# Kernel tuning notes

Hardware: AMD Instinct MI355X
Metric: run time of the kernel (lower is better)

## Reference

```python
import jax, jax.numpy as jnp
import numpy as np

N_NODES = 50000
N_EDGES = 800000
D_IN = 128
D_HID = 128
D_OUT = 128
EPS = 0.1  # GINConv eps


def setup_inputs() -> dict:
    key = jax.random.key(0)
    k = jax.random.split(key, 8)
    scale = 1.0 / np.sqrt(D_IN)
    return {
        "x": jax.random.normal(k[0], (N_NODES, D_IN), dtype=jnp.float32),
        "edge_index": jax.random.randint(k[1], (2, N_EDGES), 0, N_NODES, dtype=jnp.int64),
        "edge_weight": jax.random.uniform(k[2], (N_EDGES,), dtype=jnp.float32),
        "W1a": jax.random.normal(k[3], (D_IN, D_HID), dtype=jnp.float32) * scale,
        "W1b": jax.random.normal(k[4], (D_HID, D_HID), dtype=jnpp.float32) if False else jax.random.normal(k[4], (D_HID, D_HID), dtype=jnp.float32) * scale,
        "W2a": jax.random.normal(k[5], (D_HID, D_HID), dtype=jnp.float32) * scale,
        "W2b": jax.random.normal(k[6], (D_HID, D_OUT), dtype=jnp.float32) * scale,
    }


def _gin_conv(h, src, dst, ew, Wa, Wb, n_nodes):
    # edge-weighted neighbor sum: aggr[i] = sum_{(j->i)} w_ji * h[j]
    msg = ew[:, None] * h[src]                       # [E, d]
    aggr = jax.ops.segment_sum(msg, dst, num_segments=n_nodes)  # [N, d]
    z = (1.0 + EPS) * h + aggr                       # GIN update
    # 2-layer bias-free MLP: lin -> relu -> lin
    return jnp.maximum(z @ Wa, 0.0) @ Wb


def reference(x, edge_index, edge_weight, W1a, W1b, W2a, W2b):
    src, dst = edge_index[0], edge_index[1]
    n = x.shape[0]
    h = _gin_conv(x, src, dst, edge_weight, W1a, W1b, n)
    h = jnp.maximum(h, 0.0)  # relu between convs; dropout is identity in eval
    h = _gin_conv(h, src, dst, edge_weight, W2a, W2b, n)
    return h
```

## Files before the change

kernel.cpp:

```cpp
#include <hip/hip_runtime.h>
#include <hip/hip_fp16.h>

#define D 128
#define N_NODES 50000
#define EPSP1 1.1f

#define NPB 256
#define NBUCK 196
#define CAP 5120
#define P1E 2048
#define TS 136

typedef __attribute__((ext_vector_type(8))) short short8;
typedef __attribute__((ext_vector_type(4))) float f32x4;

__device__ __forceinline__ unsigned short f2bf(float f) {
    unsigned u = __float_as_uint(f);
    u += 0x7FFF + ((u >> 16) & 1);
    return (unsigned short)(u >> 16);
}
__device__ __forceinline__ float bf2f(unsigned short h) {
    return __uint_as_float(((unsigned)h) << 16);
}

__global__ __launch_bounds__(256) void pass1_bucket(
    const int* __restrict__ src, const int* __restrict__ dst,
    const float* __restrict__ ew, int* __restrict__ gcnt,
    uint2* __restrict__ gstage, int ne)
{
    __shared__ int bcnt[NBUCK];
    __shared__ int goff[NBUCK];
    int tid = threadIdx.x;
    int bid = blockIdx.x;
    if (tid < NBUCK) bcnt[tid] = 0;
    __syncthreads();
    int e0 = bid * P1E;
    int   rank[8];
    int   buck[8];
    uint2 pay[8];
#pragma unroll
    for (int j = 0; j < 8; ++j) {
        int e = e0 + j * 256 + tid;
        buck[j] = -1;
        if (e < ne) {
            int d_ = dst[e];
            int b  = d_ >> 8;
            int dl = d_ & 255;
            pay[j].x = (unsigned)(src[e] & 0xFFFF) | ((unsigned)dl << 16);
            pay[j].y = (unsigned)__half_as_ushort(__float2half_rn(ew[e]));
            rank[j]  = atomicAdd(&bcnt[b], 1);
            buck[j]  = b;
        }
    }
    __syncthreads();
    if (tid < NBUCK && bcnt[tid] > 0)
        goff[tid] = atomicAdd(&gcnt[tid], bcnt[tid]);
    __syncthreads();
#pragma unroll
    for (int j = 0; j < 8; ++j) {
        if (buck[j] >= 0) {
            int pos = goff[buck[j]] + rank[j];
            if (pos < CAP)
                gstage[(size_t)buck[j] * CAP + pos] = pay[j];
        }
    }
}

__global__ __launch_bounds__(512) void fused_mid(
    const uint2* __restrict__ gstage, const int* __restrict__ gcnt,
    unsigned* __restrict__ epay, int* __restrict__ off,
    const float* __restrict__ x, unsigned short* __restrict__ hb, int n4,
    const float* __restrict__ W1a, const float* __restrict__ W1b,
    const float* __restrict__ W2a, const float* __restrict__ W2b,
    unsigned short* __restrict__ wp)
{
    __shared__ int hist[NPB];
    __shared__ int scn[NPB];
    __shared__ int loc[NPB];
    __shared__ int wtot[8];
    __shared__ int base_s;
    __shared__ unsigned csr[CAP];

    int bid = blockIdx.x;
    int t = threadIdx.x;

    if (bid < NBUCK) {
        int b = bid;
        int cnt = min(gcnt[b], CAP);

        if (t < NPB) hist[t] = 0;
        __syncthreads();

        uint2 ent[CAP / 512];
#pragma unroll
        for (int it = 0; it < CAP / 512; ++it) {
            int i = it * 512 + t;
            if (i < cnt) {
                ent[it] = gstage[(size_t)b * CAP + i];
                atomicAdd(&hist[(ent[it].x >> 16) & 255], 1);
            }
        }
        __syncthreads();

        int w = t >> 6, l = t & 63;
        if (w < 4) {
            int v = hist[w * 64 + l];
#pragma unroll
            for (int dd = 1; dd < 64; dd <<= 1) {
                int u = __shfl_up(v, dd, 64);
                if (l >= dd) v += u;
            }
            scn[w * 64 + l] = v;
            if (l == 63) wtot[w] = v;
        } else if (w == 4) {
            int v = 0;
            for (int i = l; i < NBUCK; i += 64)
                if (i < b) v += min(gcnt[i], CAP);
#pragma unroll
            for (int dd = 32; dd > 0; dd >>= 1) v += __shfl_down(v, dd, 64);
            if (l == 0) base_s = v;
        }
        __syncthreads();

        if (t < NPB) {
            int pre = 0;
#pragma unroll
            for (int j = 0; j < 3; ++j) if (j < w) pre += wtot[j];
            int incl = scn[t] + pre;
            int excl = incl - hist[t];
            int node = (b << 8) + t;
            if (node <= N_NODES) off[node] = base_s + excl;
            loc[t] = excl;
        }
        __syncthreads();

#pragma unroll
        for (int it = 0; it < CAP / 512; ++it) {
            int i = it * 512 + t;
            if (i < cnt) {
                int dl = (ent[it].x >> 16) & 255;
                int p = atomicAdd(&loc[dl], 1);
                csr[p] = (ent[it].x & 0xFFFF) | (ent[it].y << 16);
            }
        }
        __syncthreads();

        for (int i = t; i < cnt; i += 512)
            epay[base_s + i] = csr[i];
    } else if (bid < NBUCK + 782) {
        int base = (bid - NBUCK) * 2048;
#pragma unroll
        for (int it = 0; it < 4; ++it) {
            int i = base + it * 512 + t;
            if (i < n4) {
                float4 v = ((const float4*)x)[i];
                ushort4 o;
                o.x = f2bf(v.x); o.y = f2bf(v.y); o.z = f2bf(v.z); o.w = f2bf(v.w);
                ((ushort4*)hb)[i] = o;
            }
        }
    } else {
        int e2 = (bid - NBUCK - 782) * 512 + t;
        int mat = e2 >> 11;
        int e   = e2 & 2047;
        const float* W = (mat == 0) ? W1a : (mat == 1) ? W1b : (mat == 2) ? W2a : W2b;
        unsigned short* Wp = wp + (size_t)mat * 16384;
        int col = e & 127;
        int kq  = e >> 7;
        short8 v;
#pragma unroll
        for (int j = 0; j < 8; ++j)
            v[j] = (short)f2bf(W[(size_t)(kq * 8 + j) * 128 + col]);
        ((short8*)Wp)[e] = v;
    }
}

__global__ __launch_bounds__(256) void gather_kernel(
    const unsigned short* __restrict__ h, const int* __restrict__ off,
    const unsigned* __restrict__ epay, unsigned short* __restrict__ z, int n_nodes)
{
    int tid = threadIdx.x;
    int node = blockIdx.x * 4 + (tid >> 6);
    if (node >= n_nodes) return;
    int lane = tid & 63;
    int qtr  = lane >> 4;
    int sub  = lane & 15;
    int beg = off[node];
    int end = off[node + 1];
    float acc[8];
#pragma unroll
    for (int c = 0; c < 8; ++c) acc[c] = 0.f;

    int i = beg;
    for (; i + 16 <= end; i += 16) {
        unsigned p0 = epay[i + qtr];
        unsigned p1 = epay[i + 4 + qtr];
        unsigned p2 = epay[i + 8 + qtr];
        unsigned p3 = epay[i + 12 + qtr];
        short8 v0 = ((const short8*)(h + (size_t)(p0 & 0xFFFF) * D))[sub];
        short8 v1 = ((const short8*)(h + (size_t)(p1 & 0xFFFF) * D))[sub];
        short8 v2 = ((const short8*)(h + (size_t)(p2 & 0xFFFF) * D))[sub];
        short8 v3 = ((const short8*)(h + (size_t)(p3 & 0xFFFF) * D))[sub];
        float w0 = __half2float(__ushort_as_half((unsigned short)(p0 >> 16)));
        float w1 = __half2float(__ushort_as_half((unsigned short)(p1 >> 16)));
        float w2 = __half2float(__ushort_as_half((unsigned short)(p2 >> 16)));
        float w3 = __half2float(__ushort_as_half((unsigned short)(p3 >> 16)));
#pragma unroll
        for (int c = 0; c < 8; ++c)
            acc[c] += w0 * bf2f((unsigned short)v0[c]) + w1 * bf2f((unsigned short)v1[c])
                    + w2 * bf2f((unsigned short)v2[c]) + w3 * bf2f((unsigned short)v3[c]);
    }
    for (; i + 8 <= end; i += 8) {
        unsigned p0 = epay[i + qtr];
        unsigned p1 = epay[i + 4 + qtr];
        short8 v0 = ((const short8*)(h + (size_t)(p0 & 0xFFFF) * D))[sub];
        short8 v1 = ((const short8*)(h + (size_t)(p1 & 0xFFFF) * D))[sub];
        float w0 = __half2float(__ushort_as_half((unsigned short)(p0 >> 16)));
        float w1 = __half2float(__ushort_as_half((unsigned short)(p1 >> 16)));
#pragma unroll
        for (int c = 0; c < 8; ++c)
            acc[c] += w0 * bf2f((unsigned short)v0[c]) + w1 * bf2f((unsigned short)v1[c]);
    }
    for (; i + qtr < end; i += 4) {
        unsigned p0 = epay[i + qtr];
        short8 v0 = ((const short8*)(h + (size_t)(p0 & 0xFFFF) * D))[sub];
        float w0 = __half2float(__ushort_as_half((unsigned short)(p0 >> 16)));
#pragma unroll
        for (int c = 0; c < 8; ++c)
            acc[c] += w0 * bf2f((unsigned short)v0[c]);
    }

#pragma unroll
    for (int c = 0; c < 8; ++c) {
        acc[c] += __shfl(acc[c], (lane + 32) & 63, 64);
        acc[c] += __shfl(acc[c], (lane + 16) & 63, 64);
    }

    if (qtr == 0) {
        short8 xv = ((const short8*)(h + (size_t)node * D))[sub];
        short8 o;
#pragma unroll
        for (int c = 0; c < 8; ++c) {
            float v = acc[c] + EPSP1 * bf2f((unsigned short)xv[c]);
            o[c] = (short)f2bf(v);
        }
        ((short8*)(z + (size_t)node * D))[sub] = o;
    }
}

template<int RELU2, int OUT_F32>
__global__ __launch_bounds__(256) void mlp_fused(
    const unsigned short* __restrict__ A,
    const unsigned short* __restrict__ WpA,
    const unsigned short* __restrict__ WpB,
    void* __restrict__ outv, int n)
{
    __shared__ unsigned short t[128 * TS];

    int tid  = threadIdx.x;
    int wave = tid >> 6;
    int lane = tid & 63;
    int quad = lane >> 4;
    int lc   = lane & 15;
    int rbase = blockIdx.x * 128 + wave * 32;
    int rloc  = wave * 32;

    const short8 zero8 = {0, 0, 0, 0, 0, 0, 0, 0};

    short8 a[2][4];
#pragma unroll
    for (int s = 0; s < 2; ++s) {
        int row = rbase + s * 16 + lc;
        const unsigned short* ap = A + (size_t)row * D;
#pragma unroll
        for (int kk = 0; kk < 4; ++kk)
            a[s][kk] = (row < n) ? *(const short8*)(ap + kk * 32 + quad * 8) : zero8;
    }

    f32x4 acc[2][8];
#pragma unroll
    for (int s = 0; s < 2; ++s)
#pragma unroll
        for (int c = 0; c < 8; ++c)
            acc[s][c] = (f32x4){0.f, 0.f, 0.f, 0.f};

#pragma unroll
    for (int cf = 0; cf < 8; ++cf) {
        short8 b[4];
#pragma unroll
        for (int kk = 0; kk < 4; ++kk)
            b[kk] = *(const short8*)(WpA + ((size_t)(kk * 4 + quad) * 128 + cf * 16 + lc) * 8);
#pragma unroll
        for (int kk = 0; kk < 4; ++kk) {
            acc[0][cf] = __builtin_amdgcn_mfma_f32_16x16x32_bf16(a[0][kk], b[kk], acc[0][cf], 0, 0, 0);
            acc[1][cf] = __builtin_amdgcn_mfma_f32_16x16x32_bf16(a[1][kk], b[kk], acc[1][cf], 0, 0, 0);
        }
    }

#pragma unroll
    for (int s = 0; s < 2; ++s)
#pragma unroll
        for (int reg = 0; reg < 4; ++reg) {
            int row = rloc + s * 16 + quad * 4 + reg;
#pragma unroll
            for (int cf = 0; cf < 8; ++cf)
                t[row * TS + cf * 16 + lc] = f2bf(fmaxf(acc[s][cf][reg], 0.f));
        }
    __syncthreads();

#pragma unroll
    for (int s = 0; s < 2; ++s) {
        int row = rloc + s * 16 + lc;
#pragma unroll
        for (int kk = 0; kk < 4; ++kk)
            a[s][kk] = *(const short8*)&t[row * TS + kk * 32 + quad * 8];
    }
#pragma unroll
    for (int s = 0; s < 2; ++s)
#pragma unroll
        for (int c = 0; c < 8; ++c)
            acc[s][c] = (f32x4){0.f, 0.f, 0.f, 0.f};

#pragma unroll
    for (int cf = 0; cf < 8; ++cf) {
        short8 b[4];
#pragma unroll
        for (int kk = 0; kk < 4; ++kk)
            b[kk] = *(const short8*)(WpB + ((size_t)(kk * 4 + quad) * 128 + cf * 16 + lc) * 8);
#pragma unroll
        for (int kk = 0; kk < 4; ++kk) {
            acc[0][cf] = __builtin_amdgcn_mfma_f32_16x16x32_bf16(a[0][kk], b[kk], acc[0][cf], 0, 0, 0);
            acc[1][cf] = __builtin_amdgcn_mfma_f32_16x16x32_bf16(a[1][kk], b[kk], acc[1][cf], 0, 0, 0);
        }
    }

#pragma unroll
    for (int s = 0; s < 2; ++s)
#pragma unroll
        for (int reg = 0; reg < 4; ++reg) {
            int row = rbase + s * 16 + quad * 4 + reg;
            if (row < n) {
#pragma unroll
                for (int cf = 0; cf < 8; ++cf) {
                    float v = acc[s][cf][reg];
                    if (RELU2) v = fmaxf(v, 0.f);
                    int col = cf * 16 + lc;
                    if (OUT_F32)
                        ((float*)outv)[(size_t)row * D + col] = v;
                    else
                        ((unsigned short*)outv)[(size_t)row * D + col] = f2bf(v);
                }
            }
        }
}

extern "C" void kernel_launch(void* const* d_in, const int* in_sizes, int n_in,
                              void* d_out, int out_size, void* d_ws, size_t ws_size,
                              hipStream_t stream) {
    const float* x   = (const float*)d_in[0];
    const int*   ei  = (const int*)d_in[1];
    const float* ew  = (const float*)d_in[2];
    const float* W1a = (const float*)d_in[3];
    const float* W1b = (const float*)d_in[4];
    const float* W2a = (const float*)d_in[5];
    const float* W2b = (const float*)d_in[6];
    float* out = (float*)d_out;

    int n_edges = in_sizes[2];
    const int* src = ei;
    const int* dst = ei + n_edges;

    size_t node_elems = (size_t)N_NODES * D;
    unsigned short* hb = (unsigned short*)d_ws;
    unsigned short* zb = hb + node_elems;
    unsigned short* wp = zb + node_elems;
    unsigned* epay = (unsigned*)(wp + 4 * 16384);
    uint2*  gstage = (uint2*)(epay + n_edges);
    int*    gcnt   = (int*)(gstage + (size_t)NBUCK * CAP);
    int*    off    = gcnt + NBUCK;

    int p1grid = (n_edges + P1E - 1) / P1E;
    int ggrid  = (N_NODES + 127) / 128;
    int agrid  = (N_NODES + 3) / 4;
    int n4     = (int)(node_elems / 4);

    hipMemsetAsync(gcnt, 0, NBUCK * sizeof(int), stream);

    pass1_bucket<<<p1grid, 256, 0, stream>>>(src, dst, ew, gcnt, gstage, n_edges);

    fused_mid<<<NBUCK + 782 + 16, 512, 0, stream>>>(
        gstage, gcnt, epay, off,
        x, hb, n4, W1a, W1b, W2a, W2b, wp);

    unsigned short* wp0 = wp;
    unsigned short* wp1 = wp + 16384;
    unsigned short* wp2 = wp + 2 * 16384;
    unsigned short* wp3 = wp + 3 * 16384;

    gather_kernel<<<agrid, 256, 0, stream>>>(hb, off, epay, zb, N_NODES);
    mlp_fused<1, 0><<<ggrid, 256, 0, stream>>>(zb, wp0, wp1, hb, N_NODES);

    gather_kernel<<<agrid, 256, 0, stream>>>(hb, off, epay, zb, N_NODES);
    mlp_fused<0, 1><<<ggrid, 256, 0, stream>>>(zb, wp2, wp3, out, N_NODES);
}
```

Measured before the change: 201.4 us.

## Rebalance preprocessing work across bucketing and CSR kernels, drop gather x16 unroll

Moves the weight packing and about half of the x-to-bf16 conversion into the first bucketing kernel, so that independent work runs alongside the edge bucketing. The second kernel converts the remaining half alongside the CSR build, which evens out the load between the two launches. It also removes the 16-edge unrolled loop in the gather kernel and leaves the 8-edge loop, which may lower register pressure but gives less memory-level parallelism per wave.

Result: no change. 201.4 us (+0.0%).

```diff
diff --git a/kernel.cpp b/kernel.cpp
--- a/kernel.cpp
+++ b/kernel.cpp
@@ -11,6 +11,10 @@
 #define P1E 2048
 #define TS 136
 
+#define CONV_SPLIT 800768
+#define CONVA_BLKS 782
+#define CONVB_BLKS 391
+
 typedef __attribute__((ext_vector_type(8))) short short8;
 typedef __attribute__((ext_vector_type(4))) float f32x4;
 
@@ -23,56 +27,85 @@
     return __uint_as_float(((unsigned)h) << 16);
 }
 
-__global__ __launch_bounds__(256) void pass1_bucket(
+__global__ __launch_bounds__(256) void fused_a(
     const int* __restrict__ src, const int* __restrict__ dst,
     const float* __restrict__ ew, int* __restrict__ gcnt,
-    uint2* __restrict__ gstage, int ne)
-{
-    __shared__ int bcnt[NBUCK];
-    __shared__ int goff[NBUCK];
-    int tid = threadIdx.x;
-    int bid = blockIdx.x;
-    if (tid < NBUCK) bcnt[tid] = 0;
-    __syncthreads();
-    int e0 = bid * P1E;
-    int   rank[8];
-    int   buck[8];
-    uint2 pay[8];
-#pragma unroll
-    for (int j = 0; j < 8; ++j) {
-        int e = e0 + j * 256 + tid;
-        buck[j] = -1;
-        if (e < ne) {
-            int d_ = dst[e];
-            int b  = d_ >> 8;
-            int dl = d_ & 255;
-            pay[j].x = (unsigned)(src[e] & 0xFFFF) | ((unsigned)dl << 16);
-            pay[j].y = (unsigned)__half_as_ushort(__float2half_rn(ew[e]));
-            rank[j]  = atomicAdd(&bcnt[b], 1);
-            buck[j]  = b;
-        }
-    }
-    __syncthreads();
-    if (tid < NBUCK && bcnt[tid] > 0)
-        goff[tid] = atomicAdd(&gcnt[tid], bcnt[tid]);
-    __syncthreads();
-#pragma unroll
-    for (int j = 0; j < 8; ++j) {
-        if (buck[j] >= 0) {
-            int pos = goff[buck[j]] + rank[j];
-            if (pos < CAP)
-                gstage[(size_t)buck[j] * CAP + pos] = pay[j];
-        }
-    }
-}
-
-__global__ __launch_bounds__(512) void fused_mid(
-    const uint2* __restrict__ gstage, const int* __restrict__ gcnt,
-    unsigned* __restrict__ epay, int* __restrict__ off,
+    uint2* __restrict__ gstage, int ne,
     const float* __restrict__ x, unsigned short* __restrict__ hb, int n4,
     const float* __restrict__ W1a, const float* __restrict__ W1b,
     const float* __restrict__ W2a, const float* __restrict__ W2b,
-    unsigned short* __restrict__ wp)
+    unsigned short* __restrict__ wp, int p1grid)
+{
+    int bid = blockIdx.x;
+    int tid = threadIdx.x;
+    if (bid < p1grid) {
+        __shared__ int bcnt[NBUCK];
+        __shared__ int goff[NBUCK];
+        if (tid < NBUCK) bcnt[tid] = 0;
+        __syncthreads();
+        int e0 = bid * P1E;
+        int   rank[8];
+        int   buck[8];
+        uint2 pay[8];
+#pragma unroll
+        for (int j = 0; j < 8; ++j) {
+            int e = e0 + j * 256 + tid;
+            buck[j] = -1;
+            if (e < ne) {
+                int d_ = dst[e];
+                int b  = d_ >> 8;
+                int dl = d_ & 255;
+                pay[j].x = (unsigned)(src[e] & 0xFFFF) | ((unsigned)dl << 16);
+                pay[j].y = (unsigned)__half_as_ushort(__float2half_rn(ew[e]));
+                rank[j]  = atomicAdd(&bcnt[b], 1);
+                buck[j]  = b;
+            }
+        }
+        __syncthreads();
+        if (tid < NBUCK && bcnt[tid] > 0)
+            goff[tid] = atomicAdd(&gcnt[tid], bcnt[tid]);
+        __syncthreads();
+#pragma unroll
+        for (int j = 0; j < 8; ++j) {
+            if (buck[j] >= 0) {
+                int pos = goff[buck[j]] + rank[j];
+                if (pos < CAP)
+                    gstage[(size_t)buck[j] * CAP + pos] = pay[j];
+            }
+        }
+    } else if (bid < p1grid + CONVA_BLKS) {
+        int base = (bid - p1grid) * 1024;
+        int lim = (CONV_SPLIT < n4) ? CONV_SPLIT : n4;
+#pragma unroll
+        for (int it = 0; it < 4; ++it) {
+            int i = base + it * 256 + tid;
+            if (i < lim) {
+                float4 v = ((const float4*)x)[i];
+                ushort4 o;
+                o.x = f2bf(v.x); o.y = f2bf(v.y); o.z = f2bf(v.z); o.w = f2bf(v.w);
+                ((ushort4*)hb)[i] = o;
+            }
+        }
+    } else {
+        int pb = bid - p1grid - CONVA_BLKS;
+        int mat = pb >> 3;
+        const float* W = (mat == 0) ? W1a : (mat == 1) ? W1b : (mat == 2) ? W2a : W2b;
+        unsigned short* Wp = wp + (size_t)mat * 16384;
+        int e = (pb & 7) * 256 + tid;
+        int col = e & 127;
+        int kq  = e >> 7;
+        short8 v;
+#pragma unroll
+        for (int j = 0; j < 8; ++j)
+            v[j] = (short)f2bf(W[(size_t)(kq * 8 + j) * 128 + col]);
+        ((short8*)Wp)[e] = v;
+    }
+}
+
+__global__ __launch_bounds__(512) void fused_b(
+    const uint2* __restrict__ gstage, const int* __restrict__ gcnt,
+    unsigned* __restrict__ epay, int* __restrict__ off,
+    const float* __restrict__ x, unsigned short* __restrict__ hb, int n4)
 {
     __shared__ int hist[NPB];
     __shared__ int scn[NPB];
@@ -147,8 +180,8 @@
 
         for (int i = t; i < cnt; i += 512)
             epay[base_s + i] = csr[i];
-    } else if (bid < NBUCK + 782) {
-        int base = (bid - NBUCK) * 2048;
+    } else {
+        int base = CONV_SPLIT + (bid - NBUCK) * 2048;
 #pragma unroll
         for (int it = 0; it < 4; ++it) {
             int i = base + it * 512 + t;
@@ -159,19 +192,6 @@
                 ((ushort4*)hb)[i] = o;
             }
         }
-    } else {
-        int e2 = (bid - NBUCK - 782) * 512 + t;
-        int mat = e2 >> 11;
-        int e   = e2 & 2047;
-        const float* W = (mat == 0) ? W1a : (mat == 1) ? W1b : (mat == 2) ? W2a : W2b;
-        unsigned short* Wp = wp + (size_t)mat * 16384;
-        int col = e & 127;
-        int kq  = e >> 7;
-        short8 v;
-#pragma unroll
-        for (int j = 0; j < 8; ++j)
-            v[j] = (short)f2bf(W[(size_t)(kq * 8 + j) * 128 + col]);
-        ((short8*)Wp)[e] = v;
     }
 }
 
@@ -192,24 +212,6 @@
     for (int c = 0; c < 8; ++c) acc[c] = 0.f;
 
     int i = beg;
-    for (; i + 16 <= end; i += 16) {
-        unsigned p0 = epay[i + qtr];
-        unsigned p1 = epay[i + 4 + qtr];
-        unsigned p2 = epay[i + 8 + qtr];
-        unsigned p3 = epay[i + 12 + qtr];
-        short8 v0 = ((const short8*)(h + (size_t)(p0 & 0xFFFF) * D))[sub];
-        short8 v1 = ((const short8*)(h + (size_t)(p1 & 0xFFFF) * D))[sub];
-        short8 v2 = ((const short8*)(h + (size_t)(p2 & 0xFFFF) * D))[sub];
-        short8 v3 = ((const short8*)(h + (size_t)(p3 & 0xFFFF) * D))[sub];
-        float w0 = __half2float(__ushort_as_half((unsigned short)(p0 >> 16)));
-        float w1 = __half2float(__ushort_as_half((unsigned short)(p1 >> 16)));
-        float w2 = __half2float(__ushort_as_half((unsigned short)(p2 >> 16)));
-        float w3 = __half2float(__ushort_as_half((unsigned short)(p3 >> 16)));
-#pragma unroll
-        for (int c = 0; c < 8; ++c)
-            acc[c] += w0 * bf2f((unsigned short)v0[c]) + w1 * bf2f((unsigned short)v1[c])
-                    + w2 * bf2f((unsigned short)v2[c]) + w3 * bf2f((unsigned short)v3[c]);
-    }
     for (; i + 8 <= end; i += 8) {
         unsigned p0 = epay[i + qtr];
         unsigned p1 = epay[i + 4 + qtr];
@@ -386,11 +388,12 @@
 
     hipMemsetAsync(gcnt, 0, NBUCK * sizeof(int), stream);
 
-    pass1_bucket<<<p1grid, 256, 0, stream>>>(src, dst, ew, gcnt, gstage, n_edges);
-
-    fused_mid<<<NBUCK + 782 + 16, 512, 0, stream>>>(
-        gstage, gcnt, epay, off,
-        x, hb, n4, W1a, W1b, W2a, W2b, wp);
+    fused_a<<<p1grid + CONVA_BLKS + 32, 256, 0, stream>>>(
+        src, dst, ew, gcnt, gstage, n_edges,
+        x, hb, n4, W1a, W1b, W2a, W2b, wp, p1grid);
+
+    fused_b<<<NBUCK + CONVB_BLKS, 512, 0, stream>>>(
+        gstage, gcnt, epay, off, x, hb, n4);
 
     unsigned short* wp0 = wp;
     unsigned short* wp1 = wp + 16384;
```
